# Performance work log

Hardware: AMD Instinct MI355X
Metric: run time of the kernel (lower is better)

Reference implementation:

```python
import jax, jax.numpy as jnp
import numpy as np

N_HEAD = 16
N_EMBD = 1024


def setup_inputs() -> dict:
    key = jax.random.key(0)
    k1, k2, k3 = jax.random.split(key, 3)
    B, T = 2, 2048
    x = jax.random.normal(k1, (B, T, N_EMBD), dtype=jnp.float32)
    w_attn = jax.random.normal(k2, (N_EMBD, 3 * N_EMBD), dtype=jnp.float32) * 0.02
    b_attn = jnp.zeros((3 * N_EMBD,), dtype=jnp.float32)
    w_proj = jax.random.normal(k3, (N_EMBD, N_EMBD), dtype=jnp.float32) * 0.02
    b_proj = jnp.zeros((N_EMBD,), dtype=jnp.float32)
    return {"x": x, "w_attn": w_attn, "b_attn": b_attn, "w_proj": w_proj, "b_proj": b_proj}


def _split_heads(t):
    # [B, T, E] -> [B, H, T, hd]
    B, T, E = t.shape
    return t.reshape(B, T, N_HEAD, E // N_HEAD).transpose(0, 2, 1, 3)


def reference(x, w_attn, b_attn, w_proj, b_proj):
    B, T, E = x.shape
    hd = E // N_HEAD
    c = x @ w_attn + b_attn                       # [B, T, 3E]
    q, k, v = jnp.split(c, 3, axis=2)
    q, k, v = _split_heads(q), _split_heads(k), _split_heads(v)  # [B,H,T,hd]
    present = jnp.stack((k, v), axis=1)           # [B, 2, H, T, hd]
    # scores, scaled by rsqrt(head_dim)
    w = jnp.einsum("bhqd,bhkd->bhqk", q, k) * jax.lax.rsqrt(jnp.float32(hd))
    # causal mask: w * mask + -1e9 * (1 - mask)  (faithful to the source)
    mask = jnp.tril(jnp.ones((T, T), dtype=w.dtype))[None, None]
    w = w * mask + (-1e9) * (1.0 - mask)
    w = jax.nn.softmax(w, axis=-1)
    a = jnp.einsum("bhqk,bhkd->bhqd", w, v)       # [B,H,T,hd]
    a = a.transpose(0, 2, 1, 3).reshape(B, T, E)  # merge heads
    a = a @ w_proj + b_proj
    return a, present
```

## Files before the change

kernel.cpp:

```cpp
#include <hip/hip_runtime.h>

typedef unsigned short u16b;
typedef __attribute__((ext_vector_type(4))) float f32x4;
typedef __attribute__((ext_vector_type(8))) short bf16x8;

#define GLD_LDS(g, l) __builtin_amdgcn_global_load_lds( \
    (__attribute__((address_space(1))) void*)(g), \
    (__attribute__((address_space(3))) void*)(l), 16, 0, 0)

__device__ __forceinline__ u16b f2bf(float f) {
    unsigned u = __builtin_bit_cast(unsigned, f);
    u += 0x7fffu + ((u >> 16) & 1u);
    return (u16b)(u >> 16);
}
__device__ __forceinline__ unsigned trunc_bf(float f) {
    return __builtin_bit_cast(unsigned, f) >> 16;
}

__global__ void prep(const float* __restrict__ x, u16b* __restrict__ xb,
                     const float* __restrict__ w_attn, u16b* __restrict__ wab,
                     const float* __restrict__ w_proj, u16b* __restrict__ wpb) {
    __shared__ float tile[32][33];
    const int blk = blockIdx.x;
    if (blk < 4096) {
        int i = blk * 256 + threadIdx.x;
        float4 v = ((const float4*)x)[i];
        uint2 o;
        o.x = (unsigned)f2bf(v.x) | ((unsigned)f2bf(v.y) << 16);
        o.y = (unsigned)f2bf(v.z) | ((unsigned)f2bf(v.w) << 16);
        ((uint2*)xb)[i] = o;
        return;
    }
    const float* in;
    u16b* out;
    int idx, N;
    if (blk < 7168) { idx = blk - 4096; N = 3072; in = w_attn; out = wab; }
    else            { idx = blk - 7168; N = 1024; in = w_proj; out = wpb; }
    const int K = 1024;
    int kt = (idx & 31) * 32, nt = (idx >> 5) * 32;
    int c = threadIdx.x & 31, r8 = threadIdx.x >> 5;
    for (int i = 0; i < 4; i++) {
        int r = r8 + i * 8;
        tile[r][c] = in[(size_t)(kt + r) * N + nt + c];
    }
    __syncthreads();
    for (int i = 0; i < 4; i++) {
        int r = r8 + i * 8;
        out[(size_t)(nt + r) * K + kt + c] = f2bf(tile[c][r]);
    }
}

template<int EPI, int MI, int NI>
__global__ __launch_bounds__(256, 2) void gemm_bt(
    const u16b* __restrict__ A, const u16b* __restrict__ Bt,
    int M, int N, int K,
    const float* __restrict__ bias,
    float* __restrict__ out_f,
    u16b* __restrict__ q_ws, u16b* __restrict__ k_ws, u16b* __restrict__ v_t)
{
    __shared__ u16b sA[(MI * 32) * 64];
    __shared__ u16b sB[(NI * 32) * 64];
    const int tid = threadIdx.x;
    const int l = tid & 63, w = tid >> 6;
    const int lr = l & 15, lg = l >> 4;
    const int m0 = blockIdx.y * (MI * 32), n0 = blockIdx.x * (NI * 32);
    const int wm = (w >> 1) * (MI * 16), wn = (w & 1) * (NI * 16);
    f32x4 acc[MI][NI] = {};

    for (int kt = 0; kt < K; kt += 64) {
        #pragma unroll
        for (int i = 0; i < MI; i++) {
            int chunk = i * 256 + tid;
            int row = chunk >> 3;
            int cb = (chunk & 7) ^ (row & 7);
            GLD_LDS(A + (size_t)(m0 + row) * K + kt + cb * 8, &sA[(i * 256 + w * 64) * 8]);
        }
        #pragma unroll
        for (int i = 0; i < NI; i++) {
            int chunk = i * 256 + tid;
            int row = chunk >> 3;
            int cb = (chunk & 7) ^ (row & 7);
            GLD_LDS(Bt + (size_t)(n0 + row) * K + kt + cb * 8, &sB[(i * 256 + w * 64) * 8]);
        }
        __syncthreads();
        #pragma unroll
        for (int ks = 0; ks < 2; ks++) {
            bf16x8 af[MI], bf[NI];
            #pragma unroll
            for (int i = 0; i < MI; i++) {
                int arow = wm + i * 16 + lr;
                af[i] = *(const bf16x8*)((const char*)sA + arow * 128 + ((ks * 64 + lg * 16) ^ ((arow & 7) << 4)));
            }
            #pragma unroll
            for (int i = 0; i < NI; i++) {
                int brow = wn + i * 16 + lr;
                bf[i] = *(const bf16x8*)((const char*)sB + brow * 128 + ((ks * 64 + lg * 16) ^ ((brow & 7) << 4)));
            }
            #pragma unroll
            for (int mi = 0; mi < MI; mi++)
                #pragma unroll
                for (int ni = 0; ni < NI; ni++)
                    acc[mi][ni] = __builtin_amdgcn_mfma_f32_16x16x32_bf16(af[mi], bf[ni], acc[mi][ni], 0, 0, 0);
        }
        __syncthreads();
    }

    if (EPI == 1) {
        #pragma unroll
        for (int ni = 0; ni < NI; ni++) {
            int col = n0 + wn + ni * 16 + lr;
            float bv = bias[col];
            #pragma unroll
            for (int mi = 0; mi < MI; mi++)
                #pragma unroll
                for (int jj = 0; jj < 4; jj++) {
                    int rowm = m0 + wm + mi * 16 + lg * 4 + jj;
                    out_f[(size_t)rowm * N + col] = acc[mi][ni][jj] + bv;
                }
        }
    } else {
        const int qkv = n0 >> 10;
        #pragma unroll
        for (int ni = 0; ni < NI; ni++) {
            int n = n0 + wn + ni * 16 + lr;
            float bv = bias[n];
            int h = (n >> 6) & 15, d = n & 63;
            #pragma unroll
            for (int mi = 0; mi < MI; mi++) {
                const int mbase = m0 + wm + mi * 16 + lg * 4;
                const int b = mbase >> 11, tb = mbase & 2047;
                float cv[4];
                #pragma unroll
                for (int jj = 0; jj < 4; jj++)
                    cv[jj] = acc[mi][ni][jj] + bv;
                if (qkv == 0) {
                    #pragma unroll
                    for (int jj = 0; jj < 4; jj++)
                        q_ws[((size_t)(b * 16 + h) * 2048 + tb + jj) * 64 + d] =
                            f2bf(cv[jj] * 0.18033688011f);
                } else if (qkv == 1) {
                    #pragma unroll
                    for (int jj = 0; jj < 4; jj++) {
                        out_f[((size_t)((b * 2 + 0) * 16 + h) * 2048 + tb + jj) * 64 + d] = cv[jj];
                        k_ws[((size_t)(b * 16 + h) * 2048 + tb + jj) * 64 + d] = f2bf(cv[jj]);
                    }
                } else {
                    #pragma unroll
                    for (int jj = 0; jj < 4; jj++)
                        out_f[((size_t)((b * 2 + 1) * 16 + h) * 2048 + tb + jj) * 64 + d] = cv[jj];
                    uint2 pk;
                    pk.x = (unsigned)f2bf(cv[0]) | ((unsigned)f2bf(cv[1]) << 16);
                    pk.y = (unsigned)f2bf(cv[2]) | ((unsigned)f2bf(cv[3]) << 16);
                    *(uint2*)(v_t + ((size_t)((b * 16 + h) * 64 + d)) * 2048 + tb) = pk;
                }
            }
        }
    }
}

__global__ __launch_bounds__(256, 4) void attn_fwd(
    const u16b* __restrict__ q_ws, const u16b* __restrict__ k_ws,
    const u16b* __restrict__ v_t, u16b* __restrict__ a_ws)
{
    __shared__ u16b sK[2][64 * 64];
    __shared__ u16b sV[2][64 * 64];
    __shared__ u16b sP[4][16 * 64];
    const int tid = threadIdx.x;
    const int l = tid & 63, w = tid >> 6;
    const int lr = l & 15, lg = l >> 4;
    const int g = blockIdx.x >> 5, bh = blockIdx.x & 31;
    const int a = g & 7, bq = g >> 3;
    const int qt = (bq == 0) ? a : (bq == 1) ? 15 - a : (bq == 2) ? 16 + a : 31 - a;
    const int b = bh >> 4, h = bh & 15;
    const size_t kbase = (size_t)bh * 2048 * 64;
    const size_t vbase = (size_t)bh * 64 * 2048;

    const int chunk0 = tid, chunk1 = 256 + tid;
    const int row0 = chunk0 >> 3, cb0 = (chunk0 & 7) ^ (row0 & 7);
    const int row1 = chunk1 >> 3, cb1 = (chunk1 & 7) ^ (row1 & 7);
    const u16b* kp0 = k_ws + kbase + (size_t)row0 * 64 + cb0 * 8;
    const u16b* kp1 = k_ws + kbase + (size_t)row1 * 64 + cb1 * 8;
    const u16b* vp0 = v_t + vbase + (size_t)row0 * 2048 + cb0 * 8;
    const u16b* vp1 = v_t + vbase + (size_t)row1 * 2048 + cb1 * 8;

    bf16x8 qf[2];
    {
        const u16b* qp = q_ws + kbase + (size_t)(qt * 64 + w * 16 + lr) * 64 + lg * 8;
        qf[0] = *(const bf16x8*)qp;
        qf[1] = *(const bf16x8*)(qp + 32);
    }
    const bf16x8 ones = {0x3F80, 0x3F80, 0x3F80, 0x3F80, 0x3F80, 0x3F80, 0x3F80, 0x3F80};
    f32x4 Oacc[4] = {};
    f32x4 Lacc = {};

    GLD_LDS(kp0, &sK[0][chunk0 * 8]);
    GLD_LDS(kp1, &sK[0][chunk1 * 8]);
    GLD_LDS(vp0, &sV[0][chunk0 * 8]);
    GLD_LDS(vp1, &sV[0][chunk1 * 8]);
    __syncthreads();
    int cur = 0;

    #pragma unroll 1
    for (int j = 0; j <= qt; j++) {
        if (j < qt) {
            int nxt = cur ^ 1;
            size_t ko = (size_t)(j + 1) * 64 * 64;
            size_t vo = (size_t)(j + 1) * 64;
            GLD_LDS(kp0 + ko, &sK[nxt][chunk0 * 8]);
            GLD_LDS(kp1 + ko, &sK[nxt][chunk1 * 8]);
            GLD_LDS(vp0 + vo, &sV[nxt][chunk0 * 8]);
            GLD_LDS(vp1 + vo, &sV[nxt][chunk1 * 8]);
        }
        const u16b* cK = &sK[cur][0];
        const u16b* cV = &sV[cur][0];

        f32x4 S[4];
        __builtin_amdgcn_s_setprio(1);
        #pragma unroll
        for (int c = 0; c < 4; c++) {
            f32x4 s = {};
            #pragma unroll
            for (int ks = 0; ks < 2; ks++) {
                int krow = c * 16 + lr;
                bf16x8 kf = *(const bf16x8*)((const char*)cK + krow * 128 + ((ks * 64 + lg * 16) ^ ((krow & 7) << 4)));
                s = __builtin_amdgcn_mfma_f32_16x16x32_bf16(kf, qf[ks], s, 0, 0, 0);
            }
            S[c] = s;
        }
        __builtin_amdgcn_s_setprio(0);
        if (j == qt) {
            const int ql = w * 16 + lr;
            #pragma unroll
            for (int c = 0; c < 4; c++)
                #pragma unroll
                for (int jj = 0; jj < 4; jj++)
                    if (c * 16 + lg * 4 + jj > ql) S[c][jj] = -1e9f;
        }
        u16b* myP = &sP[w][0];
        #pragma unroll
        for (int c = 0; c < 4; c++) {
            #pragma unroll
            for (int jj = 0; jj < 4; jj++)
                S[c][jj] = __builtin_amdgcn_exp2f(S[c][jj]);
            uint2 pk;
            pk.x = trunc_bf(S[c][0]) | (trunc_bf(S[c][1]) << 16);
            pk.y = trunc_bf(S[c][2]) | (trunc_bf(S[c][3]) << 16);
            *(uint2*)((char*)myP + lr * 128 + ((c * 32 + lg * 8) ^ ((lr & 7) << 4))) = pk;
        }
        __builtin_amdgcn_s_setprio(1);
        #pragma unroll
        for (int ks = 0; ks < 2; ks++) {
            bf16x8 pa = *(const bf16x8*)((const char*)myP + lr * 128 + ((ks * 64 + lg * 16) ^ ((lr & 7) << 4)));
            #pragma unroll
            for (int dc = 0; dc < 4; dc++) {
                int vrow = dc * 16 + lr;
                bf16x8 vb = *(const bf16x8*)((const char*)cV + vrow * 128 + ((ks * 64 + lg * 16) ^ ((vrow & 7) << 4)));
                Oacc[dc] = __builtin_amdgcn_mfma_f32_16x16x32_bf16(pa, vb, Oacc[dc], 0, 0, 0);
            }
            Lacc = __builtin_amdgcn_mfma_f32_16x16x32_bf16(pa, ones, Lacc, 0, 0, 0);
        }
        __builtin_amdgcn_s_setprio(0);
        __syncthreads();
        cur ^= 1;
    }
    #pragma unroll
    for (int jj = 0; jj < 4; jj++) {
        float inv = 1.f / Lacc[jj];
        int q = qt * 64 + w * 16 + lg * 4 + jj;
        #pragma unroll
        for (int dc = 0; dc < 4; dc++) {
            int d = dc * 16 + lr;
            a_ws[(size_t)(b * 2048 + q) * 1024 + h * 64 + d] = f2bf(Oacc[dc][jj] * inv);
        }
    }
}

extern "C" void kernel_launch(void* const* d_in, const int* in_sizes, int n_in,
                              void* d_out, int out_size, void* d_ws, size_t ws_size,
                              hipStream_t stream) {
    const float* x      = (const float*)d_in[0];
    const float* w_attn = (const float*)d_in[1];
    const float* b_attn = (const float*)d_in[2];
    const float* w_proj = (const float*)d_in[3];
    const float* b_proj = (const float*)d_in[4];
    float* out = (float*)d_out;
    float* present = out + 4194304;

    char* ws = (char*)d_ws;
    u16b* xb   = (u16b*)(ws);
    u16b* wab  = (u16b*)(ws + 8388608);
    u16b* wpb  = (u16b*)(ws + 14680064);
    u16b* q_ws = (u16b*)(ws + 16777216);
    u16b* k_ws = (u16b*)(ws + 25165824);
    u16b* v_t  = (u16b*)(ws + 33554432);
    u16b* a_ws = (u16b*)(ws + 41943040);

    prep<<<8192, 256, 0, stream>>>(x, xb, w_attn, wab, w_proj, wpb);
    gemm_bt<0, 4, 4><<<dim3(24, 32), 256, 0, stream>>>(xb, wab, 4096, 3072, 1024, b_attn,
                                                       present, q_ws, k_ws, v_t);
    attn_fwd<<<1024, 256, 0, stream>>>(q_ws, k_ws, v_t, a_ws);
    gemm_bt<1, 2, 2><<<dim3(16, 64), 256, 0, stream>>>(a_ws, wpb, 4096, 1024, 1024, b_proj,
                                                       out, nullptr, nullptr, nullptr);
}
```

Before: 100.5 us.

## Add double-buffered 256x256-tile QKV GEMM kernel with async LDS prefetch

```diff
diff --git a/kernel.cpp b/kernel.cpp
--- a/kernel.cpp
+++ b/kernel.cpp
@@ -50,13 +50,125 @@
     }
 }
 
+__global__ __launch_bounds__(1024, 4) void gemm_qkv_pipe(
+    const u16b* __restrict__ A, const u16b* __restrict__ Bt,
+    int M, int N, int K,
+    const float* __restrict__ bias,
+    float* __restrict__ out_f,
+    u16b* __restrict__ q_ws, u16b* __restrict__ k_ws, u16b* __restrict__ v_t)
+{
+    __shared__ u16b sA[2][256 * 64];
+    __shared__ u16b sB[2][256 * 64];
+    const int tid = threadIdx.x;
+    const int l = tid & 63, w = tid >> 6;
+    const int lr = l & 15, lg = l >> 4;
+    const int m0 = blockIdx.y * 256, n0 = blockIdx.x * 256;
+    const int wm = (w >> 2) * 64, wn = (w & 3) * 64;
+    f32x4 acc[4][4] = {};
+
+    int srow[2], scb[2];
+    #pragma unroll
+    for (int i = 0; i < 2; i++) {
+        int chunk = i * 1024 + tid;
+        srow[i] = chunk >> 3;
+        scb[i] = (chunk & 7) ^ (srow[i] & 7);
+    }
+
+#define STAGE_Q(buf, ktile)                                                       \
+    {                                                                             \
+        const int _kt = (ktile) * 64;                                             \
+        _Pragma("unroll")                                                         \
+        for (int i = 0; i < 2; i++) {                                             \
+            GLD_LDS(A + (size_t)(m0 + srow[i]) * K + _kt + scb[i] * 8,            \
+                    &sA[buf][(i * 1024 + tid) * 8]);                              \
+            GLD_LDS(Bt + (size_t)(n0 + srow[i]) * K + _kt + scb[i] * 8,           \
+                    &sB[buf][(i * 1024 + tid) * 8]);                              \
+        }                                                                         \
+    }
+
+    const int NT = K >> 6;
+    STAGE_Q(0, 0);
+    STAGE_Q(1, 1);
+    asm volatile("s_waitcnt vmcnt(4)" ::: "memory");
+    __builtin_amdgcn_s_barrier();
+
+    #pragma unroll 1
+    for (int t = 0; t < NT; ++t) {
+        const u16b* bAp = &sA[t & 1][0];
+        const u16b* bBp = &sB[t & 1][0];
+        #pragma unroll
+        for (int ks = 0; ks < 2; ks++) {
+            bf16x8 af[4], bf[4];
+            #pragma unroll
+            for (int i = 0; i < 4; i++) {
+                int arow = wm + i * 16 + lr;
+                af[i] = *(const bf16x8*)((const char*)bAp + arow * 128 + ((ks * 64 + lg * 16) ^ ((arow & 7) << 4)));
+                int brow = wn + i * 16 + lr;
+                bf[i] = *(const bf16x8*)((const char*)bBp + brow * 128 + ((ks * 64 + lg * 16) ^ ((brow & 7) << 4)));
+            }
+            __builtin_amdgcn_s_setprio(1);
+            #pragma unroll
+            for (int mi = 0; mi < 4; mi++)
+                #pragma unroll
+                for (int ni = 0; ni < 4; ni++)
+                    acc[mi][ni] = __builtin_amdgcn_mfma_f32_16x16x32_bf16(af[mi], bf[ni], acc[mi][ni], 0, 0, 0);
+            __builtin_amdgcn_s_setprio(0);
+        }
+        __builtin_amdgcn_s_barrier();
+        if (t + 2 < NT) {
+            STAGE_Q(t & 1, t + 2);
+            asm volatile("s_waitcnt vmcnt(4)" ::: "memory");
+        } else {
+            asm volatile("s_waitcnt vmcnt(0)" ::: "memory");
+        }
+        __builtin_amdgcn_s_barrier();
+    }
+#undef STAGE_Q
+
+    const int qkv = n0 >> 10;
+    #pragma unroll
+    for (int ni = 0; ni < 4; ni++) {
+        int n = n0 + wn + ni * 16 + lr;
+        float bv = bias[n];
+        int h = (n >> 6) & 15, d = n & 63;
+        #pragma unroll
+        for (int mi = 0; mi < 4; mi++) {
+            const int mbase = m0 + wm + mi * 16 + lg * 4;
+            const int b = mbase >> 11, tb = mbase & 2047;
+            float cv[4];
+            #pragma unroll
+            for (int jj = 0; jj < 4; jj++)
+                cv[jj] = acc[mi][ni][jj] + bv;
+            if (qkv == 0) {
+                #pragma unroll
+                for (int jj = 0; jj < 4; jj++)
+                    q_ws[((size_t)(b * 16 + h) * 2048 + tb + jj) * 64 + d] =
+                        f2bf(cv[jj] * 0.18033688011f);
+            } else if (qkv == 1) {
+                #pragma unroll
+                for (int jj = 0; jj < 4; jj++) {
+                    out_f[((size_t)((b * 2 + 0) * 16 + h) * 2048 + tb + jj) * 64 + d] = cv[jj];
+                    k_ws[((size_t)(b * 16 + h) * 2048 + tb + jj) * 64 + d] = f2bf(cv[jj]);
+                }
+            } else {
+                #pragma unroll
+                for (int jj = 0; jj < 4; jj++)
+                    out_f[((size_t)((b * 2 + 1) * 16 + h) * 2048 + tb + jj) * 64 + d] = cv[jj];
+                uint2 pk;
+                pk.x = (unsigned)f2bf(cv[0]) | ((unsigned)f2bf(cv[1]) << 16);
+                pk.y = (unsigned)f2bf(cv[2]) | ((unsigned)f2bf(cv[3]) << 16);
+                *(uint2*)(v_t + ((size_t)((b * 16 + h) * 64 + d)) * 2048 + tb) = pk;
+            }
+        }
+    }
+}
+
 template<int EPI, int MI, int NI>
 __global__ __launch_bounds__(256, 2) void gemm_bt(
     const u16b* __restrict__ A, const u16b* __restrict__ Bt,
     int M, int N, int K,
     const float* __restrict__ bias,
-    float* __restrict__ out_f,
-    u16b* __restrict__ q_ws, u16b* __restrict__ k_ws, u16b* __restrict__ v_t)
+    float* __restrict__ out_f)
 {
     __shared__ u16b sA[(MI * 32) * 64];
     __shared__ u16b sB[(NI * 32) * 64];
@@ -105,56 +217,17 @@
         __syncthreads();
     }
 
-    if (EPI == 1) {
-        #pragma unroll
-        for (int ni = 0; ni < NI; ni++) {
-            int col = n0 + wn + ni * 16 + lr;
-            float bv = bias[col];
-            #pragma unroll
-            for (int mi = 0; mi < MI; mi++)
-                #pragma unroll
-                for (int jj = 0; jj < 4; jj++) {
-                    int rowm = m0 + wm + mi * 16 + lg * 4 + jj;
-                    out_f[(size_t)rowm * N + col] = acc[mi][ni][jj] + bv;
-                }
-        }
-    } else {
-        const int qkv = n0 >> 10;
-        #pragma unroll
-        for (int ni = 0; ni < NI; ni++) {
-            int n = n0 + wn + ni * 16 + lr;
-            float bv = bias[n];
-            int h = (n >> 6) & 15, d = n & 63;
-            #pragma unroll
-            for (int mi = 0; mi < MI; mi++) {
-                const int mbase = m0 + wm + mi * 16 + lg * 4;
-                const int b = mbase >> 11, tb = mbase & 2047;
-                float cv[4];
-                #pragma unroll
-                for (int jj = 0; jj < 4; jj++)
-                    cv[jj] = acc[mi][ni][jj] + bv;
-                if (qkv == 0) {
-                    #pragma unroll
-                    for (int jj = 0; jj < 4; jj++)
-                        q_ws[((size_t)(b * 16 + h) * 2048 + tb + jj) * 64 + d] =
-                            f2bf(cv[jj] * 0.18033688011f);
-                } else if (qkv == 1) {
-                    #pragma unroll
-                    for (int jj = 0; jj < 4; jj++) {
-                        out_f[((size_t)((b * 2 + 0) * 16 + h) * 2048 + tb + jj) * 64 + d] = cv[jj];
-                        k_ws[((size_t)(b * 16 + h) * 2048 + tb + jj) * 64 + d] = f2bf(cv[jj]);
-                    }
-                } else {
-                    #pragma unroll
-                    for (int jj = 0; jj < 4; jj++)
-                        out_f[((size_t)((b * 2 + 1) * 16 + h) * 2048 + tb + jj) * 64 + d] = cv[jj];
-                    uint2 pk;
-                    pk.x = (unsigned)f2bf(cv[0]) | ((unsigned)f2bf(cv[1]) << 16);
-                    pk.y = (unsigned)f2bf(cv[2]) | ((unsigned)f2bf(cv[3]) << 16);
-                    *(uint2*)(v_t + ((size_t)((b * 16 + h) * 64 + d)) * 2048 + tb) = pk;
-                }
-            }
-        }
+    #pragma unroll
+    for (int ni = 0; ni < NI; ni++) {
+        int col = n0 + wn + ni * 16 + lr;
+        float bv = bias[col];
+        #pragma unroll
+        for (int mi = 0; mi < MI; mi++)
+            #pragma unroll
+            for (int jj = 0; jj < 4; jj++) {
+                int rowm = m0 + wm + mi * 16 + lg * 4 + jj;
+                out_f[(size_t)rowm * N + col] = acc[mi][ni][jj] + bv;
+            }
     }
 }
 
@@ -296,9 +369,9 @@
     u16b* a_ws = (u16b*)(ws + 41943040);
 
     prep<<<8192, 256, 0, stream>>>(x, xb, w_attn, wab, w_proj, wpb);
-    gemm_bt<0, 4, 4><<<dim3(24, 32), 256, 0, stream>>>(xb, wab, 4096, 3072, 1024, b_attn,
-                                                       present, q_ws, k_ws, v_t);
+    gemm_qkv_pipe<<<dim3(12, 16), 1024, 0, stream>>>(xb, wab, 4096, 3072, 1024, b_attn,
+                                                     present, q_ws, k_ws, v_t);
     attn_fwd<<<1024, 256, 0, stream>>>(q_ws, k_ws, v_t, a_ws);
     gemm_bt<1, 2, 2><<<dim3(16, 64), 256, 0, stream>>>(a_ws, wpb, 4096, 1024, 1024, b_proj,
-                                                       out, nullptr, nullptr, nullptr);
-}
+                                                       out);
+}
```

Measured after the change: 105.8 us. 5.3% more time.

## Single-buffer K/V in LDS with register prefetch to raise attention occupancy

Applied to the files above, without the earlier changes.

```diff
diff --git a/kernel.cpp b/kernel.cpp
--- a/kernel.cpp
+++ b/kernel.cpp
@@ -158,12 +158,12 @@
     }
 }
 
-__global__ __launch_bounds__(256, 4) void attn_fwd(
+__global__ __launch_bounds__(256, 6) void attn_fwd(
     const u16b* __restrict__ q_ws, const u16b* __restrict__ k_ws,
     const u16b* __restrict__ v_t, u16b* __restrict__ a_ws)
 {
-    __shared__ u16b sK[2][64 * 64];
-    __shared__ u16b sV[2][64 * 64];
+    __shared__ u16b sK[64 * 64];
+    __shared__ u16b sV[64 * 64];
     __shared__ u16b sP[4][16 * 64];
     const int tid = threadIdx.x;
     const int l = tid & 63, w = tid >> 6;
@@ -193,26 +193,30 @@
     f32x4 Oacc[4] = {};
     f32x4 Lacc = {};
 
-    GLD_LDS(kp0, &sK[0][chunk0 * 8]);
-    GLD_LDS(kp1, &sK[0][chunk1 * 8]);
-    GLD_LDS(vp0, &sV[0][chunk0 * 8]);
-    GLD_LDS(vp1, &sV[0][chunk1 * 8]);
+    {
+        uint4 k0 = *(const uint4*)kp0;
+        uint4 k1 = *(const uint4*)kp1;
+        uint4 v0 = *(const uint4*)vp0;
+        uint4 v1 = *(const uint4*)vp1;
+        *(uint4*)&sK[chunk0 * 8] = k0;
+        *(uint4*)&sK[chunk1 * 8] = k1;
+        *(uint4*)&sV[chunk0 * 8] = v0;
+        *(uint4*)&sV[chunk1 * 8] = v1;
+    }
     __syncthreads();
-    int cur = 0;
 
     #pragma unroll 1
     for (int j = 0; j <= qt; j++) {
-        if (j < qt) {
-            int nxt = cur ^ 1;
+        uint4 nk0, nk1, nv0, nv1;
+        const bool pre = (j < qt);
+        if (pre) {
             size_t ko = (size_t)(j + 1) * 64 * 64;
             size_t vo = (size_t)(j + 1) * 64;
-            GLD_LDS(kp0 + ko, &sK[nxt][chunk0 * 8]);
-            GLD_LDS(kp1 + ko, &sK[nxt][chunk1 * 8]);
-            GLD_LDS(vp0 + vo, &sV[nxt][chunk0 * 8]);
-            GLD_LDS(vp1 + vo, &sV[nxt][chunk1 * 8]);
-        }
-        const u16b* cK = &sK[cur][0];
-        const u16b* cV = &sV[cur][0];
+            nk0 = *(const uint4*)(kp0 + ko);
+            nk1 = *(const uint4*)(kp1 + ko);
+            nv0 = *(const uint4*)(vp0 + vo);
+            nv1 = *(const uint4*)(vp1 + vo);
+        }
 
         f32x4 S[4];
         __builtin_amdgcn_s_setprio(1);
@@ -222,7 +226,7 @@
             #pragma unroll
             for (int ks = 0; ks < 2; ks++) {
                 int krow = c * 16 + lr;
-                bf16x8 kf = *(const bf16x8*)((const char*)cK + krow * 128 + ((ks * 64 + lg * 16) ^ ((krow & 7) << 4)));
+                bf16x8 kf = *(const bf16x8*)((const char*)sK + krow * 128 + ((ks * 64 + lg * 16) ^ ((krow & 7) << 4)));
                 s = __builtin_amdgcn_mfma_f32_16x16x32_bf16(kf, qf[ks], s, 0, 0, 0);
             }
             S[c] = s;
@@ -254,14 +258,20 @@
             #pragma unroll
             for (int dc = 0; dc < 4; dc++) {
                 int vrow = dc * 16 + lr;
-                bf16x8 vb = *(const bf16x8*)((const char*)cV + vrow * 128 + ((ks * 64 + lg * 16) ^ ((vrow & 7) << 4)));
+                bf16x8 vb = *(const bf16x8*)((const char*)sV + vrow * 128 + ((ks * 64 + lg * 16) ^ ((vrow & 7) << 4)));
                 Oacc[dc] = __builtin_amdgcn_mfma_f32_16x16x32_bf16(pa, vb, Oacc[dc], 0, 0, 0);
             }
             Lacc = __builtin_amdgcn_mfma_f32_16x16x32_bf16(pa, ones, Lacc, 0, 0, 0);
         }
         __builtin_amdgcn_s_setprio(0);
         __syncthreads();
-        cur ^= 1;
+        if (pre) {
+            *(uint4*)&sK[chunk0 * 8] = nk0;
+            *(uint4*)&sK[chunk1 * 8] = nk1;
+            *(uint4*)&sV[chunk0 * 8] = nv0;
+            *(uint4*)&sV[chunk1 * 8] = nv1;
+        }
+        __syncthreads();
     }
     #pragma unroll
     for (int jj = 0; jj < 4; jj++) {
```

New measurement: 113.2 us. 12.7% more time.

## Replace QKV GEMM with triple-buffered 256x128 tile kernel using async LDS ring

Applied to the files above, without the earlier changes.

```diff
diff --git a/kernel.cpp b/kernel.cpp
--- a/kernel.cpp
+++ b/kernel.cpp
@@ -50,13 +50,129 @@
     }
 }
 
+__global__ __launch_bounds__(512, 1) void gemm_ring_qkv(
+    const u16b* __restrict__ A, const u16b* __restrict__ Bt,
+    int M, int N, int K,
+    const float* __restrict__ bias,
+    float* __restrict__ out_f,
+    u16b* __restrict__ q_ws, u16b* __restrict__ k_ws, u16b* __restrict__ v_t)
+{
+    __shared__ u16b sA[3][256 * 64];
+    __shared__ u16b sB[3][128 * 64];
+    const int tid = threadIdx.x;
+    const int l = tid & 63, w = tid >> 6;
+    const int lr = l & 15, lg = l >> 4;
+    const int m0 = blockIdx.y * 256, n0 = blockIdx.x * 128;
+    const int wm = (w >> 1) * 64, wn = (w & 1) * 64;
+    f32x4 acc[4][4] = {};
+
+#define STAGE_R(t)                                                                \
+    {                                                                             \
+        const int _b = (t) % 3;                                                   \
+        const int _kt = (t) << 6;                                                 \
+        _Pragma("unroll")                                                         \
+        for (int i = 0; i < 4; i++) {                                             \
+            int chunk = i * 512 + tid;                                            \
+            int row = chunk >> 3, cb = (chunk & 7) ^ (row & 7);                   \
+            GLD_LDS(A + (size_t)(m0 + row) * K + _kt + cb * 8, &sA[_b][chunk * 8]); \
+        }                                                                         \
+        _Pragma("unroll")                                                         \
+        for (int i = 0; i < 2; i++) {                                             \
+            int chunk = i * 512 + tid;                                            \
+            int row = chunk >> 3, cb = (chunk & 7) ^ (row & 7);                   \
+            GLD_LDS(Bt + (size_t)(n0 + row) * K + _kt + cb * 8, &sB[_b][chunk * 8]); \
+        }                                                                         \
+    }
+
+#define COMPUTE_R(t)                                                              \
+    {                                                                             \
+        const int _b = (t) % 3;                                                   \
+        const char* pA = (const char*)&sA[_b][0];                                 \
+        const char* pB = (const char*)&sB[_b][0];                                 \
+        _Pragma("unroll")                                                         \
+        for (int ks = 0; ks < 2; ks++) {                                          \
+            bf16x8 af[4], bf[4];                                                  \
+            _Pragma("unroll")                                                     \
+            for (int i = 0; i < 4; i++) {                                         \
+                int ar = wm + i * 16 + lr;                                        \
+                af[i] = *(const bf16x8*)(pA + ar * 128 + ((ks * 64 + lg * 16) ^ ((ar & 7) << 4))); \
+                int br = wn + i * 16 + lr;                                        \
+                bf[i] = *(const bf16x8*)(pB + br * 128 + ((ks * 64 + lg * 16) ^ ((br & 7) << 4))); \
+            }                                                                     \
+            __builtin_amdgcn_s_setprio(1);                                        \
+            _Pragma("unroll")                                                     \
+            for (int mi = 0; mi < 4; mi++)                                        \
+                _Pragma("unroll")                                                 \
+                for (int ni = 0; ni < 4; ni++)                                    \
+                    acc[mi][ni] = __builtin_amdgcn_mfma_f32_16x16x32_bf16(        \
+                        af[mi], bf[ni], acc[mi][ni], 0, 0, 0);                    \
+            __builtin_amdgcn_s_setprio(0);                                        \
+        }                                                                         \
+    }
+
+    const int NT = K >> 6;
+    STAGE_R(0);
+    STAGE_R(1);
+    asm volatile("s_waitcnt vmcnt(6)" ::: "memory");
+    __builtin_amdgcn_s_barrier();
+
+    #pragma unroll 1
+    for (int t = 0; t < NT; ++t) {
+        if (t + 2 < NT) STAGE_R(t + 2);
+        COMPUTE_R(t);
+        if (t + 1 < NT) {
+            if (t + 2 < NT) asm volatile("s_waitcnt vmcnt(6)" ::: "memory");
+            else            asm volatile("s_waitcnt vmcnt(0)" ::: "memory");
+            __builtin_amdgcn_s_barrier();
+        }
+    }
+#undef STAGE_R
+#undef COMPUTE_R
+
+    const int qkv = n0 >> 10;
+    #pragma unroll
+    for (int ni = 0; ni < 4; ni++) {
+        int n = n0 + wn + ni * 16 + lr;
+        float bv = bias[n];
+        int h = (n >> 6) & 15, d = n & 63;
+        #pragma unroll
+        for (int mi = 0; mi < 4; mi++) {
+            const int mbase = m0 + wm + mi * 16 + lg * 4;
+            const int b = mbase >> 11, tb = mbase & 2047;
+            float cv[4];
+            #pragma unroll
+            for (int jj = 0; jj < 4; jj++)
+                cv[jj] = acc[mi][ni][jj] + bv;
+            if (qkv == 0) {
+                #pragma unroll
+                for (int jj = 0; jj < 4; jj++)
+                    q_ws[((size_t)(b * 16 + h) * 2048 + tb + jj) * 64 + d] =
+                        f2bf(cv[jj] * 0.18033688011f);
+            } else if (qkv == 1) {
+                #pragma unroll
+                for (int jj = 0; jj < 4; jj++) {
+                    out_f[((size_t)((b * 2 + 0) * 16 + h) * 2048 + tb + jj) * 64 + d] = cv[jj];
+                    k_ws[((size_t)(b * 16 + h) * 2048 + tb + jj) * 64 + d] = f2bf(cv[jj]);
+                }
+            } else {
+                #pragma unroll
+                for (int jj = 0; jj < 4; jj++)
+                    out_f[((size_t)((b * 2 + 1) * 16 + h) * 2048 + tb + jj) * 64 + d] = cv[jj];
+                uint2 pk;
+                pk.x = (unsigned)f2bf(cv[0]) | ((unsigned)f2bf(cv[1]) << 16);
+                pk.y = (unsigned)f2bf(cv[2]) | ((unsigned)f2bf(cv[3]) << 16);
+                *(uint2*)(v_t + ((size_t)((b * 16 + h) * 64 + d)) * 2048 + tb) = pk;
+            }
+        }
+    }
+}
+
 template<int EPI, int MI, int NI>
 __global__ __launch_bounds__(256, 2) void gemm_bt(
     const u16b* __restrict__ A, const u16b* __restrict__ Bt,
     int M, int N, int K,
     const float* __restrict__ bias,
-    float* __restrict__ out_f,
-    u16b* __restrict__ q_ws, u16b* __restrict__ k_ws, u16b* __restrict__ v_t)
+    float* __restrict__ out_f)
 {
     __shared__ u16b sA[(MI * 32) * 64];
     __shared__ u16b sB[(NI * 32) * 64];
@@ -105,56 +221,17 @@
         __syncthreads();
     }
 
-    if (EPI == 1) {
-        #pragma unroll
-        for (int ni = 0; ni < NI; ni++) {
-            int col = n0 + wn + ni * 16 + lr;
-            float bv = bias[col];
-            #pragma unroll
-            for (int mi = 0; mi < MI; mi++)
-                #pragma unroll
-                for (int jj = 0; jj < 4; jj++) {
-                    int rowm = m0 + wm + mi * 16 + lg * 4 + jj;
-                    out_f[(size_t)rowm * N + col] = acc[mi][ni][jj] + bv;
-                }
-        }
-    } else {
-        const int qkv = n0 >> 10;
-        #pragma unroll
-        for (int ni = 0; ni < NI; ni++) {
-            int n = n0 + wn + ni * 16 + lr;
-            float bv = bias[n];
-            int h = (n >> 6) & 15, d = n & 63;
-            #pragma unroll
-            for (int mi = 0; mi < MI; mi++) {
-                const int mbase = m0 + wm + mi * 16 + lg * 4;
-                const int b = mbase >> 11, tb = mbase & 2047;
-                float cv[4];
-                #pragma unroll
-                for (int jj = 0; jj < 4; jj++)
-                    cv[jj] = acc[mi][ni][jj] + bv;
-                if (qkv == 0) {
-                    #pragma unroll
-                    for (int jj = 0; jj < 4; jj++)
-                        q_ws[((size_t)(b * 16 + h) * 2048 + tb + jj) * 64 + d] =
-                            f2bf(cv[jj] * 0.18033688011f);
-                } else if (qkv == 1) {
-                    #pragma unroll
-                    for (int jj = 0; jj < 4; jj++) {
-                        out_f[((size_t)((b * 2 + 0) * 16 + h) * 2048 + tb + jj) * 64 + d] = cv[jj];
-                        k_ws[((size_t)(b * 16 + h) * 2048 + tb + jj) * 64 + d] = f2bf(cv[jj]);
-                    }
-                } else {
-                    #pragma unroll
-                    for (int jj = 0; jj < 4; jj++)
-                        out_f[((size_t)((b * 2 + 1) * 16 + h) * 2048 + tb + jj) * 64 + d] = cv[jj];
-                    uint2 pk;
-                    pk.x = (unsigned)f2bf(cv[0]) | ((unsigned)f2bf(cv[1]) << 16);
-                    pk.y = (unsigned)f2bf(cv[2]) | ((unsigned)f2bf(cv[3]) << 16);
-                    *(uint2*)(v_t + ((size_t)((b * 16 + h) * 64 + d)) * 2048 + tb) = pk;
-                }
-            }
-        }
+    #pragma unroll
+    for (int ni = 0; ni < NI; ni++) {
+        int col = n0 + wn + ni * 16 + lr;
+        float bv = bias[col];
+        #pragma unroll
+        for (int mi = 0; mi < MI; mi++)
+            #pragma unroll
+            for (int jj = 0; jj < 4; jj++) {
+                int rowm = m0 + wm + mi * 16 + lg * 4 + jj;
+                out_f[(size_t)rowm * N + col] = acc[mi][ni][jj] + bv;
+            }
     }
 }
 
@@ -296,9 +373,9 @@
     u16b* a_ws = (u16b*)(ws + 41943040);
 
     prep<<<8192, 256, 0, stream>>>(x, xb, w_attn, wab, w_proj, wpb);
-    gemm_bt<0, 4, 4><<<dim3(24, 32), 256, 0, stream>>>(xb, wab, 4096, 3072, 1024, b_attn,
-                                                       present, q_ws, k_ws, v_t);
+    gemm_ring_qkv<<<dim3(24, 16), 512, 0, stream>>>(xb, wab, 4096, 3072, 1024, b_attn,
+                                                    present, q_ws, k_ws, v_t);
     attn_fwd<<<1024, 256, 0, stream>>>(q_ws, k_ws, v_t, a_ws);
     gemm_bt<1, 2, 2><<<dim3(16, 64), 256, 0, stream>>>(a_ws, wpb, 4096, 1024, 1024, b_proj,
-                                                       out, nullptr, nullptr, nullptr);
-}
+                                                       out);
+}
```

Result: slower. 119.9 us (+19.3%).
